# Kernel optimization log

Hardware: AMD Instinct MI355X
Metric: run time of the kernel (lower is better)

Reference implementation:

```python
import jax, jax.numpy as jnp
import numpy as np

EMBED_DIM = 1024
T1, T2, B = 2048, 2048, 4


def setup_inputs() -> dict:
    key = jax.random.key(0)
    ks = jax.random.split(key, 11)
    s = 1.0 / np.sqrt(EMBED_DIM)
    inp = {
        "x1": jax.random.normal(ks[0], (T1, B, EMBED_DIM), jnp.float32),
        "x2": jax.random.normal(ks[1], (T2, B, EMBED_DIM), jnp.float32),
        "x3": jax.random.normal(ks[2], (T2, B, EMBED_DIM), jnp.float32),
        "wq": jax.random.normal(ks[3], (EMBED_DIM, EMBED_DIM), jnp.float32) * s,
        "bq": jnp.zeros((EMBED_DIM,), jnp.float32),
        "wk": jax.random.normal(ks[4], (EMBED_DIM, EMBED_DIM), jnp.float32) * s,
        "bk": jnp.zeros((EMBED_DIM,), jnp.float32),
        "wv": jax.random.normal(ks[5], (EMBED_DIM, EMBED_DIM), jnp.float32) * s,
        "bv": jnp.zeros((EMBED_DIM,), jnp.float32),
        "wu": jax.random.normal(ks[6], (EMBED_DIM, EMBED_DIM), jnp.float32) * s,
        "bu": jnp.zeros((EMBED_DIM,), jnp.float32),
    }
    return inp


def reference(x1, x2, x3, wq, bq, wk, bk, wv, bv, wu, bu):
    # x1: [T1,B,C], x2: [T2,B,C]; x3 is unused by the original forward.
    C = x1.shape[-1]
    x1b = jnp.swapaxes(x1, 0, 1)  # [B,T1,C]
    x2b = jnp.swapaxes(x2, 0, 1)  # [B,T2,C]
    q = x1b @ wq.T + bq           # [B,T1,C]
    k = x2b @ wk.T + bk           # [B,T2,C]
    v = x2b @ wv.T + bv           # [B,T2,C]
    # single-head attention over full embed dim (num_heads unused in forward)
    scores = jnp.einsum("btc,bsc->bts", q, k) / jnp.sqrt(jnp.float32(C))
    attn = jax.nn.softmax(scores, axis=-1)  # [B,T1,T2]
    # dropout omitted (eval mode / deterministic reference)
    x = jnp.einsum("bts,bsc->btc", attn, v)  # [B,T1,C]
    x = x @ wu.T + bu
    return jnp.swapaxes(x, 0, 1)  # [T1,B,C]
```

## Files before the change

kernel.cpp:

```cpp
#include <hip/hip_runtime.h>
#include <hip/hip_bf16.h>
#include <stdint.h>

#define T1 2048
#define T2 2048
#define NB 4
#define CC 1024

typedef __attribute__((ext_vector_type(4))) float   f32x4;
typedef __attribute__((ext_vector_type(8))) __bf16  bf16x8;
typedef __attribute__((ext_vector_type(8))) unsigned short u16x8;

__device__ __forceinline__ unsigned short f2bf(float f) {
    union { float f; uint32_t u; } x; x.f = f;
    uint32_t u = x.u;
    uint32_t r = (u + 0x7fffu + ((u >> 16) & 1u)) >> 16;
    return (unsigned short)r;
}

__device__ __forceinline__ float bf2f(unsigned short b) {
    return __uint_as_float(((uint32_t)b) << 16);
}

__device__ __forceinline__ void gll16(const void* g, void* l) {
    __builtin_amdgcn_global_load_lds((const __attribute__((address_space(1))) void*)g,
                                     (__attribute__((address_space(3))) void*)l, 16, 0, 0);
}

__global__ __launch_bounds__(256) void convall_k(const float* __restrict__ wq,
                                                 const float* __restrict__ wk,
                                                 const float* __restrict__ wv,
                                                 const float* __restrict__ wu,
                                                 const float* __restrict__ x1,
                                                 const float* __restrict__ x2,
                                                 unsigned short* __restrict__ dst) {
    size_t idx = ((size_t)blockIdx.x * 256 + threadIdx.x) * 8;
    const float* s;
    size_t off;
    if (idx < 4194304) {
        int wsel = (int)(idx >> 20);
        s = (wsel == 0) ? wq : (wsel == 1) ? wk : (wsel == 2) ? wv : wu;
        off = idx & 1048575;
    } else if (idx < 12582912) {
        s = x1; off = idx - 4194304;
    } else {
        s = x2; off = idx - 12582912;
    }
    f32x4 a = *(const f32x4*)(s + off);
    f32x4 b = *(const f32x4*)(s + off + 4);
    u16x8 o;
    o[0] = f2bf(a.x); o[1] = f2bf(a.y); o[2] = f2bf(a.z); o[3] = f2bf(a.w);
    o[4] = f2bf(b.x); o[5] = f2bf(b.y); o[6] = f2bf(b.z); o[7] = f2bf(b.w);
    *(u16x8*)(dst + idx) = o;
}

enum { M_PROJQ = 0, M_KV, M_SCORES, M_PV, M_OUT };

template <int MODE, int KDIM>
__global__ __launch_bounds__(256) void gemm_bt(const unsigned short* __restrict__ Aptr,
                                               const unsigned short* __restrict__ Bptr,
                                               const float* __restrict__ bias,
                                               const float* __restrict__ bias2,
                                               void* __restrict__ Out,
                                               void* __restrict__ Out2) {
    __shared__ unsigned short As[128 * 32];
    __shared__ unsigned short Bs[128 * 32];

    const int tid  = threadIdx.x;
    const int lane = tid & 63;
    const int w    = tid >> 6;
    const int wr   = w >> 1, wc = w & 1;

    const int bid = blockIdx.x;
    const int xcd = bid & 7;
    const int i   = bid >> 3;
    int m0, n0, z = 0;
    if constexpr (MODE == M_SCORES) {
        z = xcd >> 1;
        const int mhalf = xcd & 1;
        const int nblk = i >> 3, mloc = i & 7;
        m0 = (mhalf * 8 + mloc) * 128;
        n0 = nblk * 128;
    } else if constexpr (MODE == M_PV) {
        z = xcd >> 1;
        const int nhalf = xcd & 1;
        const int nloc = i & 3, mblk = i >> 2;
        m0 = mblk * 128;
        n0 = (nhalf * 4 + nloc) * 128;
    } else if constexpr (MODE == M_KV) {
        const int mloc = i & 7, nblk = i >> 3;
        m0 = (xcd * 8 + mloc) * 128;
        n0 = nblk * 128;
    } else {
        const int mloc = i & 7, nblk = i >> 3;
        m0 = (xcd * 8 + mloc) * 128;
        n0 = nblk * 128;
    }

    size_t aoff = 0, boff = 0;
    if constexpr (MODE == M_SCORES) { aoff = (size_t)z * T1 * CC; boff = (size_t)z * T2 * CC; }
    if constexpr (MODE == M_PV)     { aoff = (size_t)z * T1 * T2; boff = (size_t)z * CC * T2; }

    const unsigned short* Ab = Aptr + aoff;
    const unsigned short* Bb = Bptr + boff;

    f32x4 acc[4][4] = {};

    const int ln15 = lane & 15;
    const int l4   = lane >> 4;
    const int srow = tid >> 2, sseg = tid & 3;

    for (int kt = 0; kt < KDIM; kt += 32) {
        __syncthreads();
#pragma unroll
        for (int p = 0; p < 2; ++p) {
            int c = p * 256 + tid;
            int row = p * 64 + srow;
            gll16(Ab + (size_t)(m0 + row) * KDIM + kt + sseg * 8, &As[c * 8]);
        }
#pragma unroll
        for (int p = 0; p < 2; ++p) {
            int c = p * 256 + tid;
            int row = p * 64 + srow;
            gll16(Bb + (size_t)(n0 + row) * KDIM + kt + sseg * 8, &Bs[c * 8]);
        }
        __syncthreads();
        bf16x8 af[4], bf[4];
#pragma unroll
        for (int i2 = 0; i2 < 4; ++i2) {
            int arow = wr * 64 + i2 * 16 + ln15;
            af[i2] = *(const bf16x8*)(&As[arow * 32 + l4 * 8]);
            int brow = wc * 64 + i2 * 16 + ln15;
            bf[i2] = *(const bf16x8*)(&Bs[brow * 32 + l4 * 8]);
        }
#pragma unroll
        for (int i2 = 0; i2 < 4; ++i2)
#pragma unroll
            for (int j = 0; j < 4; ++j)
                acc[i2][j] = __builtin_amdgcn_mfma_f32_16x16x32_bf16(af[i2], bf[j], acc[i2][j], 0, 0, 0);
    }

#pragma unroll
    for (int j = 0; j < 4; ++j) {
        const int n = n0 + wc * 64 + j * 16 + ln15;
        float bval = 0.f;
        if constexpr (MODE == M_PROJQ || MODE == M_OUT)
            bval = bias[n];
        if constexpr (MODE == M_KV)
            bval = (n < CC) ? bias[n] : bias2[n - CC];
#pragma unroll
        for (int i2 = 0; i2 < 4; ++i2) {
#pragma unroll
            for (int r = 0; r < 4; ++r) {
                const int m = m0 + wr * 64 + i2 * 16 + l4 * 4 + r;
                float val = acc[i2][j][r];
                if constexpr (MODE == M_PROJQ) {
                    unsigned short* o = (unsigned short*)Out;
                    o[(size_t)(m & 3) * (T1 * CC) + (size_t)(m >> 2) * CC + n] = f2bf(val + bval);
                } else if constexpr (MODE == M_KV) {
                    if (n < CC) {
                        unsigned short* o = (unsigned short*)Out;
                        o[(size_t)(m & 3) * (T2 * CC) + (size_t)(m >> 2) * CC + n] = f2bf(val + bval);
                    } else {
                        unsigned short* o = (unsigned short*)Out2;
                        o[(size_t)(m & 3) * (CC * T2) + (size_t)(n - CC) * T2 + (m >> 2)] = f2bf(val + bval);
                    }
                } else if constexpr (MODE == M_SCORES) {
                    unsigned short* o = (unsigned short*)Out + (size_t)z * T1 * T2;
                    o[(size_t)m * T2 + n] = f2bf(val * 0.03125f);
                } else if constexpr (MODE == M_PV) {
                    unsigned short* o = (unsigned short*)Out + (size_t)z * T1 * CC;
                    o[(size_t)m * CC + n] = f2bf(val);
                } else {
                    float* o = (float*)Out;
                    o[(size_t)(m & (T1 - 1)) * (NB * CC) + (size_t)(m >> 11) * CC + n] = val + bval;
                }
            }
        }
    }
}

__global__ __launch_bounds__(256) void softmax_k(unsigned short* __restrict__ SP) {
    const int tid = threadIdx.x, lane = tid & 63, w = tid >> 6;
    unsigned short* p = SP + (size_t)blockIdx.x * T2;
    u16x8 v = *(const u16x8*)(p + tid * 8);
    float f[8];
#pragma unroll
    for (int j = 0; j < 8; ++j) f[j] = bf2f(v[j]);
    float mx = f[0];
#pragma unroll
    for (int j = 1; j < 8; ++j) mx = fmaxf(mx, f[j]);
#pragma unroll
    for (int off = 32; off; off >>= 1) mx = fmaxf(mx, __shfl_xor(mx, off));
    __shared__ float red[8];
    if (lane == 0) red[w] = mx;
    __syncthreads();
    mx = fmaxf(fmaxf(red[0], red[1]), fmaxf(red[2], red[3]));
    float s = 0.f, e[8];
#pragma unroll
    for (int j = 0; j < 8; ++j) { e[j] = __expf(f[j] - mx); s += e[j]; }
#pragma unroll
    for (int off = 32; off; off >>= 1) s += __shfl_xor(s, off);
    if (lane == 0) red[4 + w] = s;
    __syncthreads();
    s = red[4] + red[5] + red[6] + red[7];
    float inv = 1.f / s;
    u16x8 o;
#pragma unroll
    for (int j = 0; j < 8; ++j) o[j] = f2bf(e[j] * inv);
    *(u16x8*)(p + tid * 8) = o;
}

extern "C" void kernel_launch(void* const* d_in, const int* in_sizes, int n_in,
                              void* d_out, int out_size, void* d_ws, size_t ws_size,
                              hipStream_t stream) {
    const float* x1 = (const float*)d_in[0];
    const float* x2 = (const float*)d_in[1];
    const float* wq = (const float*)d_in[3];
    const float* bq = (const float*)d_in[4];
    const float* wk = (const float*)d_in[5];
    const float* bk = (const float*)d_in[6];
    const float* wv = (const float*)d_in[7];
    const float* bv = (const float*)d_in[8];
    const float* wu = (const float*)d_in[9];
    const float* bu = (const float*)d_in[10];

    char* ws = (char*)d_ws;
    const size_t WB_OFF  = 0;
    const size_t XB1_OFF = 8388608;
    const size_t XB2_OFF = 25165824;
    const size_t SP_OFF  = 8388608;
    const size_t Q_OFF   = 41943040;
    const size_t K_OFF   = 58720256;
    const size_t V_OFF   = 75497472;
    const size_t O_OFF   = 41943040;
    const size_t WS_END  = 92274688;
    if (ws_size < WS_END) return;

    unsigned short* wb  = (unsigned short*)(ws + WB_OFF);
    unsigned short* Xb1 = (unsigned short*)(ws + XB1_OFF);
    unsigned short* Xb2 = (unsigned short*)(ws + XB2_OFF);
    unsigned short* SP  = (unsigned short*)(ws + SP_OFF);
    unsigned short* Qb  = (unsigned short*)(ws + Q_OFF);
    unsigned short* Kb  = (unsigned short*)(ws + K_OFF);
    unsigned short* Vt  = (unsigned short*)(ws + V_OFF);
    unsigned short* Ob  = (unsigned short*)(ws + O_OFF);

    convall_k<<<dim3(10240), 256, 0, stream>>>(wq, wk, wv, wu, x1, x2, wb);

    gemm_bt<M_PROJQ, 1024><<<dim3(512), 256, 0, stream>>>(Xb1, wb, bq, nullptr, Qb, nullptr);

    gemm_bt<M_KV, 1024><<<dim3(1024), 256, 0, stream>>>(Xb2, wb + 1048576, bk, bv, Kb, Vt);

    gemm_bt<M_SCORES, 1024><<<dim3(1024), 256, 0, stream>>>(Qb, Kb, nullptr, nullptr, SP, nullptr);

    softmax_k<<<dim3(8192), 256, 0, stream>>>(SP);

    gemm_bt<M_PV, 2048><<<dim3(512), 256, 0, stream>>>(SP, Vt, nullptr, nullptr, Ob, nullptr);

    gemm_bt<M_OUT, 1024><<<dim3(512), 256, 0, stream>>>(Ob, wb + 3 * 1048576, bu, nullptr, d_out, nullptr);
}
```

Measured before the change: 374.3 us.

## Double-buffer LDS tiles to overlap global loads with MFMA compute

Splits the shared-memory A/B tiles into two buffers and issues the global-to-LDS loads for the next K-tile before computing on the current one. The loop now needs one barrier per iteration instead of two, and load latency can hide behind the MFMA work. The cost is twice the LDS footprint (32KB per block), which can reduce occupancy. Correctness relies on the async gll16 loads being complete by the barrier.

```diff
diff --git a/kernel.cpp b/kernel.cpp
--- a/kernel.cpp
+++ b/kernel.cpp
@@ -63,8 +63,8 @@
                                                const float* __restrict__ bias2,
                                                void* __restrict__ Out,
                                                void* __restrict__ Out2) {
-    __shared__ unsigned short As[128 * 32];
-    __shared__ unsigned short Bs[128 * 32];
+    __shared__ unsigned short As[2][128 * 32];
+    __shared__ unsigned short Bs[2][128 * 32];
 
     const int tid  = threadIdx.x;
     const int lane = tid & 63;
@@ -104,40 +104,47 @@
     const unsigned short* Ab = Aptr + aoff;
     const unsigned short* Bb = Bptr + boff;
 
-    f32x4 acc[4][4] = {};
-
     const int ln15 = lane & 15;
     const int l4   = lane >> 4;
     const int srow = tid >> 2, sseg = tid & 3;
 
-    for (int kt = 0; kt < KDIM; kt += 32) {
-        __syncthreads();
-#pragma unroll
-        for (int p = 0; p < 2; ++p) {
-            int c = p * 256 + tid;
-            int row = p * 64 + srow;
-            gll16(Ab + (size_t)(m0 + row) * KDIM + kt + sseg * 8, &As[c * 8]);
-        }
-#pragma unroll
-        for (int p = 0; p < 2; ++p) {
-            int c = p * 256 + tid;
-            int row = p * 64 + srow;
-            gll16(Bb + (size_t)(n0 + row) * KDIM + kt + sseg * 8, &Bs[c * 8]);
-        }
-        __syncthreads();
+    const size_t ga0 = (size_t)(m0 + srow) * KDIM + sseg * 8;
+    const size_t ga1 = (size_t)(m0 + 64 + srow) * KDIM + sseg * 8;
+    const size_t gb0 = (size_t)(n0 + srow) * KDIM + sseg * 8;
+    const size_t gb1 = (size_t)(n0 + 64 + srow) * KDIM + sseg * 8;
+    const int l8 = tid * 8;
+
+    auto stage = [&](int kt, int buf) {
+        gll16(Ab + ga0 + kt, &As[buf][l8]);
+        gll16(Ab + ga1 + kt, &As[buf][2048 + l8]);
+        gll16(Bb + gb0 + kt, &Bs[buf][l8]);
+        gll16(Bb + gb1 + kt, &Bs[buf][2048 + l8]);
+    };
+
+    f32x4 acc[4][4] = {};
+    const int NT = KDIM / 32;
+
+    stage(0, 0);
+    __syncthreads();
+
+    int cur = 0;
+    for (int t = 0; t < NT; ++t) {
+        if (t + 1 < NT) stage((t + 1) * 32, cur ^ 1);
         bf16x8 af[4], bf[4];
 #pragma unroll
         for (int i2 = 0; i2 < 4; ++i2) {
             int arow = wr * 64 + i2 * 16 + ln15;
-            af[i2] = *(const bf16x8*)(&As[arow * 32 + l4 * 8]);
+            af[i2] = *(const bf16x8*)(&As[cur][arow * 32 + l4 * 8]);
             int brow = wc * 64 + i2 * 16 + ln15;
-            bf[i2] = *(const bf16x8*)(&Bs[brow * 32 + l4 * 8]);
+            bf[i2] = *(const bf16x8*)(&Bs[cur][brow * 32 + l4 * 8]);
         }
 #pragma unroll
         for (int i2 = 0; i2 < 4; ++i2)
 #pragma unroll
             for (int j = 0; j < 4; ++j)
                 acc[i2][j] = __builtin_amdgcn_mfma_f32_16x16x32_bf16(af[i2], bf[j], acc[i2][j], 0, 0, 0);
+        __syncthreads();
+        cur ^= 1;
     }
 
 #pragma unroll
```

New measurement: 397.2 us. +6.1%, slower.
